# Performance work log

Measured on AMD Instinct MI355X. Metric: run time of the kernel, lower is better.

Reference implementation:

```python
import jax, jax.numpy as jnp
import numpy as np

N_NODES = 100000
N_EDGES = 3200000
N_HID = 3
HEAD_OUT = 1024


def setup_inputs() -> dict:
    key = jax.random.key(0)
    ks = jax.random.split(key, 8)
    feat1 = jax.random.normal(ks[0], (N_NODES, 1), dtype=jnp.float32)
    feat2 = jax.random.normal(ks[1], (N_NODES, 1), dtype=jnp.float32)
    norm = jax.random.uniform(ks[2], (N_EDGES,), dtype=jnp.float32)
    src = jax.random.randint(ks[3], (N_EDGES,), 0, N_NODES, dtype=jnp.int32)
    dst = jax.random.randint(ks[4], (N_EDGES,), 0, N_NODES, dtype=jnp.int32)
    # per-layer GIN apply_func Linear(1,1): weight [n_hid,1,1], bias [n_hid,1]
    gin_w = jax.random.normal(ks[5], (N_HID, 1, 1), dtype=jnp.float32)
    gin_b = jax.random.normal(ks[6], (N_HID, 1), dtype=jnp.float32) * 0.1
    # head Linear(num_nodes, 1024), stored as [in, out]
    net_w = jax.random.normal(ks[7], (N_NODES, HEAD_OUT), dtype=jnp.float32) * (1.0 / np.sqrt(N_NODES))
    net_b = jnp.zeros((HEAD_OUT,), dtype=jnp.float32)
    return {"feat1": feat1, "feat2": feat2, "norm": norm, "src": src, "dst": dst,
            "gin_w": gin_w, "gin_b": gin_b, "net_w": net_w, "net_b": net_b}


def reference(feat1, feat2, norm, src, dst, gin_w, gin_b, net_w, net_b):
    n = feat1.shape[0]
    e_dtype = feat1.dtype
    # in-degree (same every layer); DGL mean over mailbox divides by in-degree
    deg = jax.ops.segment_sum(jnp.ones((src.shape[0],), e_dtype), dst, num_segments=n)
    inv_deg = (1.0 / jnp.maximum(deg, 1.0))[:, None]  # [N,1]

    def forward_each(feat):
        x = feat  # [N,1]
        saved = []
        for l in range(gin_w.shape[0]):
            msg = x[src] * norm[:, None]                                # gather + edge weight [E,1]
            agg = jax.ops.segment_sum(msg, dst, num_segments=n) * inv_deg  # mean aggregate [N,1]
            rst = (x + agg) @ gin_w[l].T + gin_b[l]                     # GIN: (1+eps)*x + agg, eps=0, then Linear
            saved.append(rst)                                           # forward hook captures pre-relu output
            x = jax.nn.relu(rst)
        feats = jnp.mean(jnp.stack(saved), axis=0)  # mean over layers [N,1]
        h = feats.reshape(1, -1)                    # flatten -> [1, N]
        return h @ net_w + net_b                    # [1, 1024]

    x1 = forward_each(feat1)
    x2 = forward_each(feat2)
    return jax.nn.sigmoid(jnp.sum(x1 * x2, axis=1, keepdims=True))  # [1,1]
```

## Files before the change

### kernel.cpp

```cpp
#include <hip/hip_runtime.h>
#include <math.h>

static constexpr int NN  = 100000;
static constexpr int NE  = 3200000;
static constexpr int HO  = 1024;
static constexpr int BSH = 5;
static constexpr int BMASK = 31;
static constexpr int NB  = 3125;
static constexpr int NBP = NB + 1;
static constexpr int PB  = 256;
static constexpr int CHUNK = NE / PB;
static constexpr int AT  = 512;
static constexpr int PER_A = (NB + AT - 1) / AT;
static constexpr int RPB = 50;
static constexpr int HB  = NN / RPB;
static constexpr int CAP = 2048;
static constexpr int BT  = 49;

typedef float f4v __attribute__((ext_vector_type(4)));

__device__ __forceinline__ int bucket_swz(int blk) {
    int x = blk & 7, g = blk >> 3;
    return (x < 5) ? x * 391 + g : 1955 + (x - 5) * 390 + g;
}

__global__ __launch_bounds__(AT) void partA_k(const float* __restrict__ f1,
                                              const float* __restrict__ f2,
                                              const int* __restrict__ src,
                                              const int* __restrict__ dst,
                                              const float* __restrict__ norm,
                                              int* __restrict__ loffg,
                                              uint2* __restrict__ blocked,
                                              float2* __restrict__ x0,
                                              float* __restrict__ xacc,
                                              int* __restrict__ nodeoff) {
    __shared__ int hist[NB];
    __shared__ int wt[8];
    int blk = blockIdx.x, t = threadIdx.x;
    int lane = t & 63, w = t >> 6;
    int gi = blk * AT + t;
    if (gi < NN) x0[gi] = make_float2(f1[gi], f2[gi]);
    if (blk == 0) {
        for (int i = t; i < 2 * HO; i += AT) xacc[i] = 0.f;
        if (t == 0) nodeoff[NN] = NE;
    }
    for (int i = t; i < NB; i += AT) hist[i] = 0;
    __syncthreads();
    int base = blk * CHUNK;
    for (int i = t; i < CHUNK; i += AT)
        atomicAdd(&hist[dst[base + i] >> BSH], 1);
    __syncthreads();
    int loc[PER_A]; int s = 0;
    int b0 = t * PER_A;
#pragma unroll
    for (int k = 0; k < PER_A; ++k) {
        int i = b0 + k;
        int v = (i < NB) ? hist[i] : 0;
        loc[k] = s; s += v;
    }
    int incl = s;
#pragma unroll
    for (int off = 1; off < 64; off <<= 1) {
        int v = __shfl_up(incl, off, 64);
        if (lane >= off) incl += v;
    }
    if (lane == 63) wt[w] = incl;
    __syncthreads();
    int wpre = 0;
#pragma unroll
    for (int k = 0; k < 8; ++k) if (k < w) wpre += wt[k];
    int carry = wpre + incl - s;
#pragma unroll
    for (int k = 0; k < PER_A; ++k) {
        int i = b0 + k;
        if (i < NB) {
            int e = carry + loc[k];
            loffg[blk * NBP + i] = e;
            hist[i] = e;
        }
    }
    __syncthreads();
    for (int i = t; i < CHUNK; i += AT) {
        int e = base + i;
        int d = dst[e];
        int pos = atomicAdd(&hist[d >> BSH], 1);
        blocked[base + pos] = make_uint2((unsigned)src[e] | ((unsigned)(d & BMASK) << 17),
                                         __float_as_uint(norm[e]));
    }
}

__global__ __launch_bounds__(256) void transT_k(const int* __restrict__ loffg,
                                                int* __restrict__ loffT) {
    __shared__ int tile[64][65];
    int bx = blockIdx.x % BT;
    int ky = blockIdx.x / BT;
    int tx = threadIdx.x & 63, ty = threadIdx.x >> 6;
    int b = bx * 64 + tx;
#pragma unroll
    for (int j = 0; j < 16; ++j) {
        int k = ky * 64 + ty + j * 4;
        tile[ty + j * 4][tx] = (b < NB) ? loffg[k * NBP + b] : 0;
    }
    __syncthreads();
#pragma unroll
    for (int j = 0; j < 16; ++j) {
        int row = ty + j * 4;
        int bb = bx * 64 + row;
        if (bb < NB) loffT[bb * PB + ky * 64 + tx] = tile[tx][row];
    }
}

__global__ __launch_bounds__(256) void sortB_k(const uint2* __restrict__ blocked,
                                               const int* __restrict__ loffT,
                                               uint2* __restrict__ sorted2,
                                               int* __restrict__ nodeoff) {
    __shared__ uint2 rec[CAP];
    __shared__ int wtot[4], wsum[4];
    __shared__ int cnt[32], curs[32];
    __shared__ float inv[32];
    int t = threadIdx.x;
    int lane = t & 63, w = t >> 6;
    int b = bucket_swz(blockIdx.x);
    int o0 = loffT[b * PB + t];
    int o1 = (b == NB - 1) ? CHUNK : loffT[(b + 1) * PB + t];
    int len = o1 - o0;
    if (t < 32) cnt[t] = 0;
    int incl = len;
#pragma unroll
    for (int off = 1; off < 64; off <<= 1) {
        int v = __shfl_up(incl, off, 64);
        if (lane >= off) incl += v;
    }
    int os = o0;
#pragma unroll
    for (int off = 32; off; off >>= 1) os += __shfl_xor(os, off, 64);
    if (lane == 63) wtot[w] = incl;
    if (lane == 0)  wsum[w] = os;
    __syncthreads();
    int wpre = 0, total = 0, s0 = 0;
#pragma unroll
    for (int k = 0; k < 4; ++k) {
        int tv = wtot[k];
        if (k < w) wpre += tv;
        total += tv; s0 += wsum[k];
    }
    int start = wpre + incl - len;
    if (total > CAP) total = CAP;
    {
        int lm = (len > 0) ? len - 1 : 0;
        const uint2* srcq = blocked + (size_t)t * CHUNK + o0;
        uint2 q0 = srcq[0];
        uint2 q1 = srcq[lm < 1 ? lm : 1];
        uint2 q2 = srcq[lm < 2 ? lm : 2];
        uint2 q3 = srcq[lm < 3 ? lm : 3];
        uint2 q4 = srcq[lm < 4 ? lm : 4];
        uint2 q5 = srcq[lm < 5 ? lm : 5];
        uint2 q6 = srcq[lm < 6 ? lm : 6];
        uint2 q7 = srcq[lm < 7 ? lm : 7];
        if (len > 0 && start + 0 < CAP) rec[start + 0] = q0;
        if (len > 1 && start + 1 < CAP) rec[start + 1] = q1;
        if (len > 2 && start + 2 < CAP) rec[start + 2] = q2;
        if (len > 3 && start + 3 < CAP) rec[start + 3] = q3;
        if (len > 4 && start + 4 < CAP) rec[start + 4] = q4;
        if (len > 5 && start + 5 < CAP) rec[start + 5] = q5;
        if (len > 6 && start + 6 < CAP) rec[start + 6] = q6;
        if (len > 7 && start + 7 < CAP) rec[start + 7] = q7;
        for (int j = 8; j < len; ++j)
            if (start + j < CAP) rec[start + j] = srcq[j];
    }
    __syncthreads();
    for (int i = t; i < total; i += 256)
        atomicAdd(&cnt[(rec[i].x >> 17) & BMASK], 1);
    __syncthreads();
    if (t < 32) {
        int c = cnt[t];
        int ic = c;
#pragma unroll
        for (int off = 1; off < 32; off <<= 1) {
            int v = __shfl_up(ic, off, 32);
            if (t >= off) ic += v;
        }
        curs[t] = ic - c;
        inv[t] = 1.0f / fmaxf((float)c, 1.0f);
        nodeoff[(b << BSH) + t] = s0 + ic - c;
    }
    __syncthreads();
    for (int i = t; i < total; i += 256) {
        uint2 r = rec[i];
        int lo = (r.x >> 17) & BMASK;
        int pos = atomicAdd(&curs[lo], 1);
        sorted2[(size_t)s0 + pos] = make_uint2(r.x & 131071u,
                               __float_as_uint(__uint_as_float(r.y) * inv[lo]));
    }
}

template<int L0>
__global__ __launch_bounds__(256) void layer_k(const uint2* __restrict__ s2,
                                               const int* __restrict__ noff,
                                               const float2* __restrict__ xin,
                                               float2* __restrict__ xout,
                                               float2* __restrict__ ssum,
                                               const float* __restrict__ gw,
                                               const float* __restrict__ gb, int l) {
    int gid = blockIdx.x * 256 + threadIdx.x;
    int node = gid >> 3, r = gid & 7;
    if (node >= NN) return;
    int i0 = noff[node], i1 = noff[node + 1];
    float ax = 0.f, ay = 0.f;
    int i = i0 + r;
    while (i + 24 < i1) {
        uint2 a0 = s2[i], a1 = s2[i + 8], a2 = s2[i + 16], a3 = s2[i + 24];
        float2 xa = xin[a0.x], xb = xin[a1.x], xc = xin[a2.x], xd = xin[a3.x];
        ax = fmaf(xa.x, __uint_as_float(a0.y), ax); ay = fmaf(xa.y, __uint_as_float(a0.y), ay);
        ax = fmaf(xb.x, __uint_as_float(a1.y), ax); ay = fmaf(xb.y, __uint_as_float(a1.y), ay);
        ax = fmaf(xc.x, __uint_as_float(a2.y), ax); ay = fmaf(xc.y, __uint_as_float(a2.y), ay);
        ax = fmaf(xd.x, __uint_as_float(a3.y), ax); ay = fmaf(xd.y, __uint_as_float(a3.y), ay);
        i += 32;
    }
    for (; i < i1; i += 8) {
        uint2 a = s2[i];
        float2 xx = xin[a.x];
        float wv = __uint_as_float(a.y);
        ax = fmaf(xx.x, wv, ax); ay = fmaf(xx.y, wv, ay);
    }
#pragma unroll
    for (int off = 1; off < 8; off <<= 1) {
        ax += __shfl_xor(ax, off, 64);
        ay += __shfl_xor(ay, off, 64);
    }
    if (r == 0) {
        float wv = gw[l], bb = gb[l];
        float2 xv = xin[node];
        float rx = fmaf(xv.x + ax, wv, bb);
        float ry = fmaf(xv.y + ay, wv, bb);
        if (L0) ssum[node] = make_float2(rx, ry);
        else { float2 s = ssum[node]; ssum[node] = make_float2(s.x + rx, s.y + ry); }
        xout[node] = make_float2(fmaxf(rx, 0.f), fmaxf(ry, 0.f));
    }
}

__global__ __launch_bounds__(256) void head_k(const float2* __restrict__ ssum,
                                              const float* __restrict__ W,
                                              float* __restrict__ part) {
    __shared__ float sf0[RPB], sf1[RPB];
    int r0 = blockIdx.x * RPB;
    int t = threadIdx.x;
    const float sc = 1.0f / 3.0f;
    if (t < RPB) {
        float2 s = ssum[r0 + t];
        sf0[t] = s.x * sc;
        sf1[t] = s.y * sc;
    }
    __syncthreads();
    float ax1=0.f, ay1=0.f, az1=0.f, aw1=0.f;
    float ax2=0.f, ay2=0.f, az2=0.f, aw2=0.f;
    int j0 = t * 4;
    const f4v* Wp = reinterpret_cast<const f4v*>(W + (size_t)r0 * HO + j0);
#pragma unroll 5
    for (int k = 0; k < RPB; ++k) {
        f4v w4 = __builtin_nontemporal_load(Wp);
        Wp += HO / 4;
        float f1 = sf0[k], f2 = sf1[k];
        ax1 = fmaf(f1, w4.x, ax1); ay1 = fmaf(f1, w4.y, ay1);
        az1 = fmaf(f1, w4.z, az1); aw1 = fmaf(f1, w4.w, aw1);
        ax2 = fmaf(f2, w4.x, ax2); ay2 = fmaf(f2, w4.y, ay2);
        az2 = fmaf(f2, w4.z, az2); aw2 = fmaf(f2, w4.w, aw2);
    }
    float* pp = part + (size_t)blockIdx.x * 2048;
    pp[j0]   = ax1; pp[j0+1] = ay1; pp[j0+2] = az1; pp[j0+3] = aw1;
    pp[1024+j0]   = ax2; pp[1024+j0+1] = ay2;
    pp[1024+j0+2] = az2; pp[1024+j0+3] = aw2;
}

__global__ __launch_bounds__(256) void reduce_k(const float* __restrict__ part,
                                                float* __restrict__ xacc) {
    int gid = blockIdx.x * 256 + threadIdx.x;
    int j = gid & 2047;
    int seg = gid >> 11;
    int b0 = (seg * HB) >> 5, b1 = ((seg + 1) * HB) >> 5;
    float s = 0.f;
    for (int b = b0; b < b1; ++b) s += part[(size_t)b * 2048 + j];
    atomicAdd(&xacc[j], s);
}

__global__ void final_k(const float* __restrict__ xacc, const float* __restrict__ nb,
                        float* __restrict__ out) {
    __shared__ float red[256];
    int t = threadIdx.x;
    float v = 0.f;
    for (int j = t; j < HO; j += 256)
        v += (xacc[j] + nb[j]) * (xacc[HO + j] + nb[j]);
    red[t] = v;
    __syncthreads();
    for (int s = 128; s > 0; s >>= 1) {
        if (t < s) red[t] += red[t + s];
        __syncthreads();
    }
    if (t == 0) out[0] = 1.0f / (1.0f + expf(-red[0]));
}

extern "C" void kernel_launch(void* const* d_in, const int* in_sizes, int n_in,
                              void* d_out, int out_size, void* d_ws, size_t ws_size,
                              hipStream_t stream) {
    const float* feat1 = (const float*)d_in[0];
    const float* feat2 = (const float*)d_in[1];
    const float* norm  = (const float*)d_in[2];
    const int*   src   = (const int*)  d_in[3];
    const int*   dst   = (const int*)  d_in[4];
    const float* gin_w = (const float*)d_in[5];
    const float* gin_b = (const float*)d_in[6];
    const float* net_w = (const float*)d_in[7];
    const float* net_b = (const float*)d_in[8];
    float* out = (float*)d_out;

    char* p = (char*)d_ws;
    uint2* blocked = (uint2*)p;               p += (size_t)NE * 8;
    float* part    = (float*)blocked;
    uint2* sorted2 = (uint2*)p;               p += (size_t)NE * 8;
    int*   loffg   = (int*)p;                 p += (size_t)PB * NBP * 4;
    int*   loffT   = (int*)p;                 p += (size_t)NB * PB * 4;
    int*   nodeoff = (int*)p;                 p += ((size_t)(NN + 1) * 4 + 15) & ~15ull;
    float2* x0     = (float2*)p;              p += (size_t)NN * 8;
    float2* x1     = (float2*)p;              p += (size_t)NN * 8;
    float2* ssum   = (float2*)p;              p += (size_t)NN * 8;
    float* xacc    = (float*)p;               p += (size_t)2 * HO * 4;

    int lg = (NN * 8 + 255) / 256;

    partA_k<<<PB, AT, 0, stream>>>(feat1, feat2, src, dst, norm, loffg, blocked,
                                   x0, xacc, nodeoff);
    transT_k<<<BT * 4, 256, 0, stream>>>(loffg, loffT);
    sortB_k<<<NB, 256, 0, stream>>>(blocked, loffT, sorted2, nodeoff);

    layer_k<1><<<lg, 256, 0, stream>>>(sorted2, nodeoff, x0, x1, ssum, gin_w, gin_b, 0);
    layer_k<0><<<lg, 256, 0, stream>>>(sorted2, nodeoff, x1, x0, ssum, gin_w, gin_b, 1);
    layer_k<0><<<lg, 256, 0, stream>>>(sorted2, nodeoff, x0, x1, ssum, gin_w, gin_b, 2);

    head_k<<<HB, 256, 0, stream>>>(ssum, net_w, part);
    reduce_k<<<256, 256, 0, stream>>>(part, xacc);
    final_k<<<1, 256, 0, stream>>>(xacc, net_b, out);
}
```

Baseline: 226.8 us.

## Fuse whole pipeline into one cooperative persistent kernel with grid syncs

Replaces the nine separate kernel launches with a single cooperative kernel of 256 blocks x 512 threads that runs partition, transpose, bucket sort, three GIN layers, head GEMV, reduce and final sigmoid, separated by grid.sync. The aim is to remove launch overhead and inter-kernel gaps. In exchange, the bucket-sort and layer phases now run on a fixed grid of 256 blocks using grid-stride loops, which lowers parallelism, and each grid barrier adds its own cost. The old multi-kernel path stays as a fallback if the cooperative launch fails.

```diff
diff --git a/kernel.cpp b/kernel.cpp
--- a/kernel.cpp
+++ b/kernel.cpp
@@ -1,5 +1,8 @@
 #include <hip/hip_runtime.h>
+#include <hip/hip_cooperative_groups.h>
 #include <math.h>
+
+namespace cg = cooperative_groups;
 
 static constexpr int NN  = 100000;
 static constexpr int NE  = 3200000;
@@ -8,20 +11,305 @@
 static constexpr int BMASK = 31;
 static constexpr int NB  = 3125;
 static constexpr int NBP = NB + 1;
-static constexpr int PB  = 256;
-static constexpr int CHUNK = NE / PB;
+static constexpr int GRID = 256;
 static constexpr int AT  = 512;
+static constexpr int CHUNK = NE / GRID;
 static constexpr int PER_A = (NB + AT - 1) / AT;
-static constexpr int RPB = 50;
-static constexpr int HB  = NN / RPB;
+static constexpr int RPB = 100;
+static constexpr int HU  = NN / RPB;
 static constexpr int CAP = 2048;
 static constexpr int BT  = 49;
+static constexpr int LANES = NN * 8;
+static constexpr int STRIDE = GRID * AT;
+static constexpr int RPB_F = 50;
+static constexpr int HB_F  = NN / RPB_F;
 
 typedef float f4v __attribute__((ext_vector_type(4)));
 
 __device__ __forceinline__ int bucket_swz(int blk) {
     int x = blk & 7, g = blk >> 3;
     return (x < 5) ? x * 391 + g : 1955 + (x - 5) * 390 + g;
+}
+
+__global__ __launch_bounds__(AT, 2) void mega_k(
+    const float* __restrict__ f1, const float* __restrict__ f2,
+    const int* __restrict__ src, const int* __restrict__ dst,
+    const float* __restrict__ norm,
+    const float* __restrict__ gw, const float* __restrict__ gb,
+    const float* __restrict__ W, const float* __restrict__ nbias,
+    float* __restrict__ out,
+    uint2* __restrict__ blocked, uint2* __restrict__ sorted2,
+    int* __restrict__ loffg, int* __restrict__ loffT,
+    int* __restrict__ nodeoff,
+    float2* __restrict__ x0, float2* __restrict__ x1,
+    float2* __restrict__ ssum, float* __restrict__ xacc,
+    float* __restrict__ part)
+{
+    __shared__ __align__(16) unsigned char smem[17056];
+    cg::grid_group grid = cg::this_grid();
+    int blk = blockIdx.x, t = threadIdx.x;
+    int lane = t & 63, w = t >> 6;
+
+    {
+        int* hist = (int*)smem;
+        int* wt   = hist + NB;
+        int gi = blk * AT + t;
+        if (gi < NN) x0[gi] = make_float2(f1[gi], f2[gi]);
+        if (gi < 2 * HO) xacc[gi] = 0.f;
+        if (gi == 0) nodeoff[NN] = NE;
+        for (int i = t; i < NB; i += AT) hist[i] = 0;
+        __syncthreads();
+        int base = blk * CHUNK;
+        for (int i = t; i < CHUNK; i += AT)
+            atomicAdd(&hist[dst[base + i] >> BSH], 1);
+        __syncthreads();
+        int loc[PER_A]; int s = 0;
+        int b0 = t * PER_A;
+#pragma unroll
+        for (int k = 0; k < PER_A; ++k) {
+            int i = b0 + k;
+            int v = (i < NB) ? hist[i] : 0;
+            loc[k] = s; s += v;
+        }
+        int incl = s;
+#pragma unroll
+        for (int off = 1; off < 64; off <<= 1) {
+            int v = __shfl_up(incl, off, 64);
+            if (lane >= off) incl += v;
+        }
+        if (lane == 63) wt[w] = incl;
+        __syncthreads();
+        int wpre = 0;
+#pragma unroll
+        for (int k = 0; k < 8; ++k) if (k < w) wpre += wt[k];
+        int carry = wpre + incl - s;
+#pragma unroll
+        for (int k = 0; k < PER_A; ++k) {
+            int i = b0 + k;
+            if (i < NB) {
+                int e = carry + loc[k];
+                loffg[blk * NBP + i] = e;
+                hist[i] = e;
+            }
+        }
+        __syncthreads();
+        for (int i = t; i < CHUNK; i += AT) {
+            int e = base + i;
+            int d = dst[e];
+            int pos = atomicAdd(&hist[d >> BSH], 1);
+            blocked[base + pos] = make_uint2((unsigned)src[e] | ((unsigned)(d & BMASK) << 17),
+                                             __float_as_uint(norm[e]));
+        }
+    }
+    grid.sync();
+
+    if (blk < BT * 4) {
+        int* tile = (int*)smem;
+        int bx = blk % BT, ky = blk / BT;
+        int tx = t & 63, ty = t >> 6;
+        int b = bx * 64 + tx;
+#pragma unroll
+        for (int j = 0; j < 8; ++j) {
+            int kl = ty + j * 8;
+            tile[kl * 65 + tx] = (b < NB) ? loffg[(ky * 64 + kl) * NBP + b] : 0;
+        }
+        __syncthreads();
+#pragma unroll
+        for (int j = 0; j < 8; ++j) {
+            int row = ty + j * 8;
+            int bb = bx * 64 + row;
+            if (bb < NB) loffT[(size_t)bb * GRID + ky * 64 + tx] = tile[tx * 65 + row];
+        }
+    }
+    grid.sync();
+
+    {
+        uint2* rec  = (uint2*)smem;
+        int*  wtot = (int*)(smem + 16384);
+        int*  wsum = wtot + 8;
+        int*  cnt  = wsum + 8;
+        int*  curs = cnt + 32;
+        float* inv = (float*)(curs + 32);
+        for (int b = blk; b < NB; b += GRID) {
+            __syncthreads();
+            if (t < 32) cnt[t] = 0;
+            bool valid = t < GRID;
+            int o0 = valid ? loffT[(size_t)b * GRID + t] : 0;
+            int o1 = valid ? ((b == NB - 1) ? CHUNK : loffT[(size_t)(b + 1) * GRID + t]) : 0;
+            int len = o1 - o0;
+            int incl = len;
+#pragma unroll
+            for (int off = 1; off < 64; off <<= 1) {
+                int v = __shfl_up(incl, off, 64);
+                if (lane >= off) incl += v;
+            }
+            int os = o0;
+#pragma unroll
+            for (int off = 32; off; off >>= 1) os += __shfl_xor(os, off, 64);
+            if (lane == 63) wtot[w] = incl;
+            if (lane == 0)  wsum[w] = os;
+            __syncthreads();
+            int wpre = 0, total = 0, s0 = 0;
+#pragma unroll
+            for (int k = 0; k < 8; ++k) {
+                int tv = wtot[k];
+                if (k < w) wpre += tv;
+                total += tv; s0 += wsum[k];
+            }
+            int start = wpre + incl - len;
+            if (total > CAP) total = CAP;
+            if (len > 0) {
+                const uint2* srcq = blocked + (size_t)t * CHUNK + o0;
+                int lm = len - 1;
+                uint2 q0 = srcq[0];
+                uint2 q1 = srcq[lm < 1 ? lm : 1];
+                uint2 q2 = srcq[lm < 2 ? lm : 2];
+                uint2 q3 = srcq[lm < 3 ? lm : 3];
+                if (start + 0 < CAP) rec[start + 0] = q0;
+                if (len > 1 && start + 1 < CAP) rec[start + 1] = q1;
+                if (len > 2 && start + 2 < CAP) rec[start + 2] = q2;
+                if (len > 3 && start + 3 < CAP) rec[start + 3] = q3;
+                for (int j = 4; j < len; ++j)
+                    if (start + j < CAP) rec[start + j] = srcq[j];
+            }
+            __syncthreads();
+            for (int i = t; i < total; i += AT)
+                atomicAdd(&cnt[(rec[i].x >> 17) & BMASK], 1);
+            __syncthreads();
+            if (t < 32) {
+                int c = cnt[t];
+                int ic = c;
+#pragma unroll
+                for (int off = 1; off < 32; off <<= 1) {
+                    int v = __shfl_up(ic, off, 32);
+                    if (t >= off) ic += v;
+                }
+                curs[t] = ic - c;
+                inv[t] = 1.0f / fmaxf((float)c, 1.0f);
+                nodeoff[(b << BSH) + t] = s0 + ic - c;
+            }
+            __syncthreads();
+            for (int i = t; i < total; i += AT) {
+                uint2 r = rec[i];
+                int lo = (r.x >> 17) & BMASK;
+                int pos = atomicAdd(&curs[lo], 1);
+                sorted2[(size_t)s0 + pos] = make_uint2(r.x & 131071u,
+                                   __float_as_uint(__uint_as_float(r.y) * inv[lo]));
+            }
+        }
+    }
+    grid.sync();
+
+    {
+        const float2* xi = x0;
+        float2* xo = x1;
+        for (int l = 0; l < 3; ++l) {
+            float wv = gw[l], bb = gb[l];
+            for (int gid = blk * AT + t; gid < LANES; gid += STRIDE) {
+                int node = gid >> 3, r = gid & 7;
+                int i0 = nodeoff[node], i1 = nodeoff[node + 1];
+                float ax = 0.f, ay = 0.f;
+                int i = i0 + r;
+                while (i + 24 < i1) {
+                    uint2 a0 = sorted2[i], a1 = sorted2[i + 8];
+                    uint2 a2 = sorted2[i + 16], a3 = sorted2[i + 24];
+                    float2 xa = xi[a0.x], xb = xi[a1.x], xc = xi[a2.x], xd = xi[a3.x];
+                    ax = fmaf(xa.x, __uint_as_float(a0.y), ax); ay = fmaf(xa.y, __uint_as_float(a0.y), ay);
+                    ax = fmaf(xb.x, __uint_as_float(a1.y), ax); ay = fmaf(xb.y, __uint_as_float(a1.y), ay);
+                    ax = fmaf(xc.x, __uint_as_float(a2.y), ax); ay = fmaf(xc.y, __uint_as_float(a2.y), ay);
+                    ax = fmaf(xd.x, __uint_as_float(a3.y), ax); ay = fmaf(xd.y, __uint_as_float(a3.y), ay);
+                    i += 32;
+                }
+                for (; i < i1; i += 8) {
+                    uint2 a = sorted2[i];
+                    float2 xx = xi[a.x];
+                    float ww = __uint_as_float(a.y);
+                    ax = fmaf(xx.x, ww, ax); ay = fmaf(xx.y, ww, ay);
+                }
+#pragma unroll
+                for (int off = 1; off < 8; off <<= 1) {
+                    ax += __shfl_xor(ax, off, 64);
+                    ay += __shfl_xor(ay, off, 64);
+                }
+                if (r == 0) {
+                    float2 xv = xi[node];
+                    float rx = fmaf(xv.x + ax, wv, bb);
+                    float ry = fmaf(xv.y + ay, wv, bb);
+                    if (l == 0) ssum[node] = make_float2(rx, ry);
+                    else { float2 s = ssum[node]; ssum[node] = make_float2(s.x + rx, s.y + ry); }
+                    xo[node] = make_float2(fmaxf(rx, 0.f), fmaxf(ry, 0.f));
+                }
+            }
+            grid.sync();
+            const float2* tmp = xi; xi = xo; xo = (float2*)tmp;
+        }
+    }
+
+    {
+        float* fs = (float*)smem;
+        int sub = t >> 8, tl = t & 255;
+        float* sf0 = fs + sub * 512;
+        float* sf1 = sf0 + 256;
+        for (int u0 = blk * 2; u0 < HU; u0 += GRID * 2) {
+            int unit = u0 + sub;
+            __syncthreads();
+            if (tl < RPB) {
+                float2 sv = ssum[unit * RPB + tl];
+                sf0[tl] = sv.x * (1.0f / 3.0f);
+                sf1[tl] = sv.y * (1.0f / 3.0f);
+            }
+            __syncthreads();
+            float ax1 = 0.f, ay1 = 0.f, az1 = 0.f, aw1 = 0.f;
+            float ax2 = 0.f, ay2 = 0.f, az2 = 0.f, aw2 = 0.f;
+            int j0 = tl * 4;
+            const f4v* Wp = reinterpret_cast<const f4v*>(W + (size_t)unit * RPB * HO + j0);
+#pragma unroll 5
+            for (int k = 0; k < RPB; ++k) {
+                f4v w4 = __builtin_nontemporal_load(Wp);
+                Wp += HO / 4;
+                float v1 = sf0[k], v2 = sf1[k];
+                ax1 = fmaf(v1, w4.x, ax1); ay1 = fmaf(v1, w4.y, ay1);
+                az1 = fmaf(v1, w4.z, az1); aw1 = fmaf(v1, w4.w, aw1);
+                ax2 = fmaf(v2, w4.x, ax2); ay2 = fmaf(v2, w4.y, ay2);
+                az2 = fmaf(v2, w4.z, az2); aw2 = fmaf(v2, w4.w, aw2);
+            }
+            float* pp = part + (size_t)unit * 2048;
+            pp[j0] = ax1; pp[j0+1] = ay1; pp[j0+2] = az1; pp[j0+3] = aw1;
+            pp[1024+j0] = ax2; pp[1024+j0+1] = ay2;
+            pp[1024+j0+2] = az2; pp[1024+j0+3] = aw2;
+        }
+    }
+    grid.sync();
+
+    {
+        int gid = blk * AT + t;
+        if (gid < 65536) {
+            int j = gid & 2047;
+            int seg = gid >> 11;
+            int b0 = (seg * HU) >> 5, b1 = ((seg + 1) * HU) >> 5;
+            float s = 0.f;
+            for (int b = b0; b < b1; ++b) s += part[(size_t)b * 2048 + j];
+            atomicAdd(&xacc[j], s);
+        }
+    }
+    grid.sync();
+
+    if (blk == 0) {
+        float v = 0.f;
+        for (int j = t; j < HO; j += AT)
+            v += (xacc[j] + nbias[j]) * (xacc[HO + j] + nbias[j]);
+#pragma unroll
+        for (int off = 32; off; off >>= 1) v += __shfl_xor(v, off, 64);
+        float* red = (float*)smem;
+        if (lane == 0) red[w] = v;
+        __syncthreads();
+        if (t == 0) {
+            float s = 0.f;
+#pragma unroll
+            for (int k = 0; k < 8; ++k) s += red[k];
+            out[0] = 1.0f / (1.0f + expf(-s));
+        }
+    }
 }
 
 __global__ __launch_bounds__(AT) void partA_k(const float* __restrict__ f1,
@@ -106,7 +394,7 @@
     for (int j = 0; j < 16; ++j) {
         int row = ty + j * 4;
         int bb = bx * 64 + row;
-        if (bb < NB) loffT[bb * PB + ky * 64 + tx] = tile[tx][row];
+        if (bb < NB) loffT[(size_t)bb * GRID + ky * 64 + tx] = tile[tx][row];
     }
 }
 
@@ -121,8 +409,8 @@
     int t = threadIdx.x;
     int lane = t & 63, w = t >> 6;
     int b = bucket_swz(blockIdx.x);
-    int o0 = loffT[b * PB + t];
-    int o1 = (b == NB - 1) ? CHUNK : loffT[(b + 1) * PB + t];
+    int o0 = loffT[(size_t)b * GRID + t];
+    int o1 = (b == NB - 1) ? CHUNK : loffT[(size_t)(b + 1) * GRID + t];
     int len = o1 - o0;
     if (t < 32) cnt[t] = 0;
     int incl = len;
@@ -148,7 +436,8 @@
     if (total > CAP) total = CAP;
     {
         int lm = (len > 0) ? len - 1 : 0;
-        const uint2* srcq = blocked + (size_t)t * CHUNK + o0;
+        int o0c = (o0 < CHUNK - 1) ? o0 : CHUNK - 1;
+        const uint2* srcq = blocked + (size_t)t * CHUNK + o0c;
         uint2 q0 = srcq[0];
         uint2 q1 = srcq[lm < 1 ? lm : 1];
         uint2 q2 = srcq[lm < 2 ? lm : 2];
@@ -242,11 +531,11 @@
 __global__ __launch_bounds__(256) void head_k(const float2* __restrict__ ssum,
                                               const float* __restrict__ W,
                                               float* __restrict__ part) {
-    __shared__ float sf0[RPB], sf1[RPB];
-    int r0 = blockIdx.x * RPB;
+    __shared__ float sf0[RPB_F], sf1[RPB_F];
+    int r0 = blockIdx.x * RPB_F;
     int t = threadIdx.x;
     const float sc = 1.0f / 3.0f;
-    if (t < RPB) {
+    if (t < RPB_F) {
         float2 s = ssum[r0 + t];
         sf0[t] = s.x * sc;
         sf1[t] = s.y * sc;
@@ -257,14 +546,14 @@
     int j0 = t * 4;
     const f4v* Wp = reinterpret_cast<const f4v*>(W + (size_t)r0 * HO + j0);
 #pragma unroll 5
-    for (int k = 0; k < RPB; ++k) {
+    for (int k = 0; k < RPB_F; ++k) {
         f4v w4 = __builtin_nontemporal_load(Wp);
         Wp += HO / 4;
-        float f1 = sf0[k], f2 = sf1[k];
-        ax1 = fmaf(f1, w4.x, ax1); ay1 = fmaf(f1, w4.y, ay1);
-        az1 = fmaf(f1, w4.z, az1); aw1 = fmaf(f1, w4.w, aw1);
-        ax2 = fmaf(f2, w4.x, ax2); ay2 = fmaf(f2, w4.y, ay2);
-        az2 = fmaf(f2, w4.z, az2); aw2 = fmaf(f2, w4.w, aw2);
+        float v1 = sf0[k], v2 = sf1[k];
+        ax1 = fmaf(v1, w4.x, ax1); ay1 = fmaf(v1, w4.y, ay1);
+        az1 = fmaf(v1, w4.z, az1); aw1 = fmaf(v1, w4.w, aw1);
+        ax2 = fmaf(v2, w4.x, ax2); ay2 = fmaf(v2, w4.y, ay2);
+        az2 = fmaf(v2, w4.z, az2); aw2 = fmaf(v2, w4.w, aw2);
     }
     float* pp = part + (size_t)blockIdx.x * 2048;
     pp[j0]   = ax1; pp[j0+1] = ay1; pp[j0+2] = az1; pp[j0+3] = aw1;
@@ -277,7 +566,7 @@
     int gid = blockIdx.x * 256 + threadIdx.x;
     int j = gid & 2047;
     int seg = gid >> 11;
-    int b0 = (seg * HB) >> 5, b1 = ((seg + 1) * HB) >> 5;
+    int b0 = (seg * HB_F) >> 5, b1 = ((seg + 1) * HB_F) >> 5;
     float s = 0.f;
     for (int b = b0; b < b1; ++b) s += part[(size_t)b * 2048 + j];
     atomicAdd(&xacc[j], s);
@@ -317,26 +606,40 @@
     uint2* blocked = (uint2*)p;               p += (size_t)NE * 8;
     float* part    = (float*)blocked;
     uint2* sorted2 = (uint2*)p;               p += (size_t)NE * 8;
-    int*   loffg   = (int*)p;                 p += (size_t)PB * NBP * 4;
-    int*   loffT   = (int*)p;                 p += (size_t)NB * PB * 4;
+    int*   loffg   = (int*)p;                 p += (size_t)GRID * NBP * 4;
+    int*   loffT   = (int*)p;                 p += (size_t)NB * GRID * 4;
     int*   nodeoff = (int*)p;                 p += ((size_t)(NN + 1) * 4 + 15) & ~15ull;
     float2* x0     = (float2*)p;              p += (size_t)NN * 8;
     float2* x1     = (float2*)p;              p += (size_t)NN * 8;
     float2* ssum   = (float2*)p;              p += (size_t)NN * 8;
     float* xacc    = (float*)p;               p += (size_t)2 * HO * 4;
 
+    int occ = 0;
+    hipError_t qe = hipOccupancyMaxActiveBlocksPerMultiprocessor(&occ, mega_k, AT, 0);
+    bool coop = (qe == hipSuccess && occ >= 1);
+
+    if (coop) {
+        void* args[] = {
+            (void*)&feat1, (void*)&feat2, (void*)&src, (void*)&dst, (void*)&norm,
+            (void*)&gin_w, (void*)&gin_b, (void*)&net_w, (void*)&net_b, (void*)&out,
+            (void*)&blocked, (void*)&sorted2, (void*)&loffg, (void*)&loffT,
+            (void*)&nodeoff, (void*)&x0, (void*)&x1, (void*)&ssum, (void*)&xacc,
+            (void*)&part
+        };
+        hipError_t le = hipLaunchCooperativeKernel((const void*)mega_k, dim3(GRID),
+                                                   dim3(AT), args, 0, stream);
+        if (le == hipSuccess) return;
+    }
+
     int lg = (NN * 8 + 255) / 256;
-
-    partA_k<<<PB, AT, 0, stream>>>(feat1, feat2, src, dst, norm, loffg, blocked,
-                                   x0, xacc, nodeoff);
+    partA_k<<<GRID, AT, 0, stream>>>(feat1, feat2, src, dst, norm, loffg, blocked,
+                                     x0, xacc, nodeoff);
     transT_k<<<BT * 4, 256, 0, stream>>>(loffg, loffT);
     sortB_k<<<NB, 256, 0, stream>>>(blocked, loffT, sorted2, nodeoff);
-
     layer_k<1><<<lg, 256, 0, stream>>>(sorted2, nodeoff, x0, x1, ssum, gin_w, gin_b, 0);
     layer_k<0><<<lg, 256, 0, stream>>>(sorted2, nodeoff, x1, x0, ssum, gin_w, gin_b, 1);
     layer_k<0><<<lg, 256, 0, stream>>>(sorted2, nodeoff, x0, x1, ssum, gin_w, gin_b, 2);
-
-    head_k<<<HB, 256, 0, stream>>>(ssum, net_w, part);
+    head_k<<<HB_F, 256, 0, stream>>>(ssum, net_w, part);
     reduce_k<<<256, 256, 0, stream>>>(part, xacc);
     final_k<<<1, 256, 0, stream>>>(xacc, net_b, out);
 }
```

New measurement: 526.1 us. 132% more time.

## Pack edge records into 32-bit words with quantized weights and padded buckets

Applied to the files above, without the earlier changes.

Sorted edge records shrink from 8 bytes (index + float weight) to a single 32-bit word holding a 17-bit source index and a 15-bit fixed-point normalized weight. Each node's edge list is padded to a multiple of four and buckets get fixed-stride slots, so the layer kernels can issue 16-byte vector loads and read start/end from an int2 offset array. This cuts memory traffic in the three aggregation passes and removes the global offset sum in the sort kernel. The cost is reduced weight precision (about 3e-5 absolute) and zero-padding writes, plus the risk of overflow if a bucket exceeds the fixed stride.

```diff
diff --git a/kernel.cpp b/kernel.cpp
--- a/kernel.cpp
+++ b/kernel.cpp
@@ -9,13 +9,14 @@
 static constexpr int NB  = 3125;
 static constexpr int NBP = NB + 1;
 static constexpr int PB  = 256;
+static constexpr int AT  = 512;
 static constexpr int CHUNK = NE / PB;
-static constexpr int AT  = 512;
 static constexpr int PER_A = (NB + AT - 1) / AT;
 static constexpr int RPB = 50;
 static constexpr int HB  = NN / RPB;
 static constexpr int CAP = 2048;
 static constexpr int BT  = 49;
+static constexpr int BSTRIDE = 1536;
 
 typedef float f4v __attribute__((ext_vector_type(4)));
 
@@ -32,8 +33,7 @@
                                               int* __restrict__ loffg,
                                               uint2* __restrict__ blocked,
                                               float2* __restrict__ x0,
-                                              float* __restrict__ xacc,
-                                              int* __restrict__ nodeoff) {
+                                              float* __restrict__ xacc) {
     __shared__ int hist[NB];
     __shared__ int wt[8];
     int blk = blockIdx.x, t = threadIdx.x;
@@ -42,7 +42,6 @@
     if (gi < NN) x0[gi] = make_float2(f1[gi], f2[gi]);
     if (blk == 0) {
         for (int i = t; i < 2 * HO; i += AT) xacc[i] = 0.f;
-        if (t == 0) nodeoff[NN] = NE;
     }
     for (int i = t; i < NB; i += AT) hist[i] = 0;
     __syncthreads();
@@ -106,23 +105,24 @@
     for (int j = 0; j < 16; ++j) {
         int row = ty + j * 4;
         int bb = bx * 64 + row;
-        if (bb < NB) loffT[bb * PB + ky * 64 + tx] = tile[tx][row];
+        if (bb < NB) loffT[(size_t)bb * PB + ky * 64 + tx] = tile[tx][row];
     }
 }
 
 __global__ __launch_bounds__(256) void sortB_k(const uint2* __restrict__ blocked,
                                                const int* __restrict__ loffT,
-                                               uint2* __restrict__ sorted2,
-                                               int* __restrict__ nodeoff) {
+                                               unsigned* __restrict__ s2out,
+                                               int2* __restrict__ noff) {
     __shared__ uint2 rec[CAP];
-    __shared__ int wtot[4], wsum[4];
+    __shared__ int wtot[4];
     __shared__ int cnt[32], curs[32];
     __shared__ float inv[32];
     int t = threadIdx.x;
     int lane = t & 63, w = t >> 6;
     int b = bucket_swz(blockIdx.x);
-    int o0 = loffT[b * PB + t];
-    int o1 = (b == NB - 1) ? CHUNK : loffT[(b + 1) * PB + t];
+    int gbase = b * BSTRIDE;
+    int o0 = loffT[(size_t)b * PB + t];
+    int o1 = (b == NB - 1) ? CHUNK : loffT[(size_t)(b + 1) * PB + t];
     int len = o1 - o0;
     if (t < 32) cnt[t] = 0;
     int incl = len;
@@ -131,24 +131,21 @@
         int v = __shfl_up(incl, off, 64);
         if (lane >= off) incl += v;
     }
-    int os = o0;
-#pragma unroll
-    for (int off = 32; off; off >>= 1) os += __shfl_xor(os, off, 64);
     if (lane == 63) wtot[w] = incl;
-    if (lane == 0)  wsum[w] = os;
-    __syncthreads();
-    int wpre = 0, total = 0, s0 = 0;
+    __syncthreads();
+    int wpre = 0, total = 0;
 #pragma unroll
     for (int k = 0; k < 4; ++k) {
         int tv = wtot[k];
         if (k < w) wpre += tv;
-        total += tv; s0 += wsum[k];
+        total += tv;
     }
     int start = wpre + incl - len;
     if (total > CAP) total = CAP;
     {
         int lm = (len > 0) ? len - 1 : 0;
-        const uint2* srcq = blocked + (size_t)t * CHUNK + o0;
+        int o0c = (o0 < CHUNK - 1) ? o0 : CHUNK - 1;
+        const uint2* srcq = blocked + (size_t)t * CHUNK + o0c;
         uint2 q0 = srcq[0];
         uint2 q1 = srcq[lm < 1 ? lm : 1];
         uint2 q2 = srcq[lm < 2 ? lm : 2];
@@ -174,29 +171,34 @@
     __syncthreads();
     if (t < 32) {
         int c = cnt[t];
-        int ic = c;
+        int c4 = (c + 3) & ~3;
+        int ic4 = c4;
 #pragma unroll
         for (int off = 1; off < 32; off <<= 1) {
-            int v = __shfl_up(ic, off, 32);
-            if (t >= off) ic += v;
+            int v = __shfl_up(ic4, off, 32);
+            if (t >= off) ic4 += v;
         }
-        curs[t] = ic - c;
+        int pre4 = ic4 - c4;
+        curs[t] = pre4;
         inv[t] = 1.0f / fmaxf((float)c, 1.0f);
-        nodeoff[(b << BSH) + t] = s0 + ic - c;
+        noff[(b << BSH) + t] = make_int2(gbase + pre4, gbase + pre4 + c4);
+        for (int j = c; j < c4; ++j) s2out[gbase + pre4 + j] = 0u;
     }
     __syncthreads();
     for (int i = t; i < total; i += 256) {
         uint2 r = rec[i];
         int lo = (r.x >> 17) & BMASK;
         int pos = atomicAdd(&curs[lo], 1);
-        sorted2[(size_t)s0 + pos] = make_uint2(r.x & 131071u,
-                               __float_as_uint(__uint_as_float(r.y) * inv[lo]));
+        float v = __uint_as_float(r.y) * inv[lo];
+        int q = (int)(v * 32768.f + 0.5f);
+        if (q > 32767) q = 32767;
+        s2out[gbase + pos] = (r.x & 131071u) | ((unsigned)q << 17);
     }
 }
 
 template<int L0>
-__global__ __launch_bounds__(256) void layer_k(const uint2* __restrict__ s2,
-                                               const int* __restrict__ noff,
+__global__ __launch_bounds__(256) void layer_k(const unsigned* __restrict__ s2,
+                                               const int2* __restrict__ noff,
                                                const float2* __restrict__ xin,
                                                float2* __restrict__ xout,
                                                float2* __restrict__ ssum,
@@ -205,23 +207,20 @@
     int gid = blockIdx.x * 256 + threadIdx.x;
     int node = gid >> 3, r = gid & 7;
     if (node >= NN) return;
-    int i0 = noff[node], i1 = noff[node + 1];
+    int2 no = noff[node];
+    int i0 = no.x, i1 = no.y;
     float ax = 0.f, ay = 0.f;
-    int i = i0 + r;
-    while (i + 24 < i1) {
-        uint2 a0 = s2[i], a1 = s2[i + 8], a2 = s2[i + 16], a3 = s2[i + 24];
-        float2 xa = xin[a0.x], xb = xin[a1.x], xc = xin[a2.x], xd = xin[a3.x];
-        ax = fmaf(xa.x, __uint_as_float(a0.y), ax); ay = fmaf(xa.y, __uint_as_float(a0.y), ay);
-        ax = fmaf(xb.x, __uint_as_float(a1.y), ax); ay = fmaf(xb.y, __uint_as_float(a1.y), ay);
-        ax = fmaf(xc.x, __uint_as_float(a2.y), ax); ay = fmaf(xc.y, __uint_as_float(a2.y), ay);
-        ax = fmaf(xd.x, __uint_as_float(a3.y), ax); ay = fmaf(xd.y, __uint_as_float(a3.y), ay);
-        i += 32;
-    }
-    for (; i < i1; i += 8) {
-        uint2 a = s2[i];
-        float2 xx = xin[a.x];
-        float wv = __uint_as_float(a.y);
-        ax = fmaf(xx.x, wv, ax); ay = fmaf(xx.y, wv, ay);
+    const float qs = 1.0f / 32768.0f;
+    for (int i = i0 + 4 * r; i < i1; i += 32) {
+        uint4 q = *reinterpret_cast<const uint4*>(s2 + i);
+        float2 xa = xin[q.x & 131071u]; float wa = (float)(q.x >> 17) * qs;
+        float2 xb = xin[q.y & 131071u]; float wb = (float)(q.y >> 17) * qs;
+        float2 xc = xin[q.z & 131071u]; float wc = (float)(q.z >> 17) * qs;
+        float2 xd = xin[q.w & 131071u]; float wd = (float)(q.w >> 17) * qs;
+        ax = fmaf(xa.x, wa, ax); ay = fmaf(xa.y, wa, ay);
+        ax = fmaf(xb.x, wb, ax); ay = fmaf(xb.y, wb, ay);
+        ax = fmaf(xc.x, wc, ax); ay = fmaf(xc.y, wc, ay);
+        ax = fmaf(xd.x, wd, ax); ay = fmaf(xd.y, wd, ay);
     }
 #pragma unroll
     for (int off = 1; off < 8; off <<= 1) {
@@ -260,11 +259,11 @@
     for (int k = 0; k < RPB; ++k) {
         f4v w4 = __builtin_nontemporal_load(Wp);
         Wp += HO / 4;
-        float f1 = sf0[k], f2 = sf1[k];
-        ax1 = fmaf(f1, w4.x, ax1); ay1 = fmaf(f1, w4.y, ay1);
-        az1 = fmaf(f1, w4.z, az1); aw1 = fmaf(f1, w4.w, aw1);
-        ax2 = fmaf(f2, w4.x, ax2); ay2 = fmaf(f2, w4.y, ay2);
-        az2 = fmaf(f2, w4.z, az2); aw2 = fmaf(f2, w4.w, aw2);
+        float v1 = sf0[k], v2 = sf1[k];
+        ax1 = fmaf(v1, w4.x, ax1); ay1 = fmaf(v1, w4.y, ay1);
+        az1 = fmaf(v1, w4.z, az1); aw1 = fmaf(v1, w4.w, aw1);
+        ax2 = fmaf(v2, w4.x, ax2); ay2 = fmaf(v2, w4.y, ay2);
+        az2 = fmaf(v2, w4.z, az2); aw2 = fmaf(v2, w4.w, aw2);
     }
     float* pp = part + (size_t)blockIdx.x * 2048;
     pp[j0]   = ax1; pp[j0+1] = ay1; pp[j0+2] = az1; pp[j0+3] = aw1;
@@ -314,27 +313,27 @@
     float* out = (float*)d_out;
 
     char* p = (char*)d_ws;
-    uint2* blocked = (uint2*)p;               p += (size_t)NE * 8;
-    float* part    = (float*)blocked;
-    uint2* sorted2 = (uint2*)p;               p += (size_t)NE * 8;
-    int*   loffg   = (int*)p;                 p += (size_t)PB * NBP * 4;
-    int*   loffT   = (int*)p;                 p += (size_t)NB * PB * 4;
-    int*   nodeoff = (int*)p;                 p += ((size_t)(NN + 1) * 4 + 15) & ~15ull;
-    float2* x0     = (float2*)p;              p += (size_t)NN * 8;
-    float2* x1     = (float2*)p;              p += (size_t)NN * 8;
-    float2* ssum   = (float2*)p;              p += (size_t)NN * 8;
-    float* xacc    = (float*)p;               p += (size_t)2 * HO * 4;
+    uint2* blocked   = (uint2*)p;             p += (size_t)NE * 8;
+    float* part      = (float*)blocked;
+    unsigned* sorted2 = (unsigned*)p;         p += (size_t)NB * BSTRIDE * 4;
+    int*   loffg     = (int*)p;               p += (size_t)PB * NBP * 4;
+    int*   loffT     = (int*)p;               p += (size_t)NB * PB * 4;
+    int2*  noff      = (int2*)p;              p += (size_t)NN * 8;
+    float2* x0       = (float2*)p;            p += (size_t)NN * 8;
+    float2* x1       = (float2*)p;            p += (size_t)NN * 8;
+    float2* ssum     = (float2*)p;            p += (size_t)NN * 8;
+    float* xacc      = (float*)p;             p += (size_t)2 * HO * 4;
 
     int lg = (NN * 8 + 255) / 256;
 
     partA_k<<<PB, AT, 0, stream>>>(feat1, feat2, src, dst, norm, loffg, blocked,
-                                   x0, xacc, nodeoff);
+                                   x0, xacc);
     transT_k<<<BT * 4, 256, 0, stream>>>(loffg, loffT);
-    sortB_k<<<NB, 256, 0, stream>>>(blocked, loffT, sorted2, nodeoff);
-
-    layer_k<1><<<lg, 256, 0, stream>>>(sorted2, nodeoff, x0, x1, ssum, gin_w, gin_b, 0);
-    layer_k<0><<<lg, 256, 0, stream>>>(sorted2, nodeoff, x1, x0, ssum, gin_w, gin_b, 1);
-    layer_k<0><<<lg, 256, 0, stream>>>(sorted2, nodeoff, x0, x1, ssum, gin_w, gin_b, 2);
+    sortB_k<<<NB, 256, 0, stream>>>(blocked, loffT, sorted2, noff);
+
+    layer_k<1><<<lg, 256, 0, stream>>>(sorted2, noff, x0, x1, ssum, gin_w, gin_b, 0);
+    layer_k<0><<<lg, 256, 0, stream>>>(sorted2, noff, x1, x0, ssum, gin_w, gin_b, 1);
+    layer_k<0><<<lg, 256, 0, stream>>>(sorted2, noff, x0, x1, ssum, gin_w, gin_b, 2);
 
     head_k<<<HB, 256, 0, stream>>>(ssum, net_w, part);
     reduce_k<<<256, 256, 0, stream>>>(part, xacc);
```

After: 219.0 us. -3.5%, faster.
